# Kernel optimization log

Measured on AMD Instinct MI355X. Metric: run time of the kernel, lower is better.

## Reference

```python
import jax, jax.numpy as jnp
import numpy as np

N_NODES = 10000
N_EDGES = 160000
IN_FEAT = 1024
H_FEAT = 1024
NUM_CLASSES = 64


def setup_inputs() -> dict:
    key = jax.random.key(0)
    ks = jax.random.split(key, 8)
    h = jax.random.normal(ks[0], (N_NODES, IN_FEAT), dtype=jnp.float32)
    src = jax.random.randint(ks[1], (N_EDGES,), 0, N_NODES, dtype=jnp.int32)
    dst = jax.random.randint(ks[2], (N_EDGES,), 0, N_NODES, dtype=jnp.int32)
    # Xavier-ish scaled weights (DGL uses xavier_uniform for GraphConv)
    W1 = jax.random.normal(ks[3], (IN_FEAT, H_FEAT), dtype=jnp.float32) * (1.0 / np.sqrt(IN_FEAT))
    b1 = jnp.zeros((H_FEAT,), dtype=jnp.float32)
    W2 = jax.random.normal(ks[4], (H_FEAT, H_FEAT), dtype=jnp.float32) * (1.0 / np.sqrt(H_FEAT))
    b2 = jnp.zeros((H_FEAT,), dtype=jnp.float32)
    W3 = jax.random.normal(ks[5], (H_FEAT, NUM_CLASSES), dtype=jnp.float32) * (1.0 / np.sqrt(H_FEAT))
    b3 = jnp.zeros((NUM_CLASSES,), dtype=jnp.float32)
    return {"h": h, "src": src, "dst": dst,
            "W1": W1, "b1": b1, "W2": W2, "b2": b2, "W3": W3, "b3": b3}


def _graph_conv(src, dst, norm_src, norm_dst, x, W, b):
    """DGL GraphConv with norm='both':
    out = D_dst^{-1/2} * sum_{(u,v) in E} (D_src^{-1/2} * x)_u  @ W + b
    """
    xs = x * norm_src[:, None]                     # [N, d] scaled source feats
    msg = xs[src]                                  # [E, d] gather
    agg = jax.ops.segment_sum(msg, dst, num_segments=N_NODES)  # [N, d] scatter-add
    agg = agg * norm_dst[:, None]
    return agg @ W + b


def reference(h, src, dst, W1, b1, W2, b2, W3, b3):
    ones = jnp.ones((N_EDGES,), dtype=jnp.float32)
    deg_out = jax.ops.segment_sum(ones, src, num_segments=N_NODES)  # out-degree of src
    deg_in = jax.ops.segment_sum(ones, dst, num_segments=N_NODES)   # in-degree of dst
    norm_src = jnp.clip(deg_out, 1.0, None) ** -0.5
    norm_dst = jnp.clip(deg_in, 1.0, None) ** -0.5

    x = _graph_conv(src, dst, norm_src, norm_dst, h, W1, b1)
    x = jax.nn.relu(x)
    x = _graph_conv(src, dst, norm_src, norm_dst, x, W2, b2)
    x = jax.nn.relu(x)
    x = _graph_conv(src, dst, norm_src, norm_dst, x, W3, b3)
    return x
```

## Files before the change

### kernel.cpp

```cpp
#include <hip/hip_runtime.h>

constexpr int NN   = 10000;
constexpr int NE   = 160000;
constexpr int F    = 1024;
constexpr int C3   = 64;
constexpr int MPAD = 10240;

typedef __attribute__((ext_vector_type(8))) short short8;
typedef __attribute__((ext_vector_type(8))) unsigned short ushort8v;
typedef __attribute__((ext_vector_type(4))) float floatx4;

__device__ __forceinline__ unsigned short f2bf(float f) {
    union { float f; unsigned u; } v; v.f = f;
    unsigned r = v.u + 0x7fff + ((v.u >> 16) & 1);
    return (unsigned short)(r >> 16);
}
__device__ __forceinline__ float bf2f(unsigned short u) {
    union { unsigned u; float f; } v; v.u = ((unsigned)u) << 16;
    return v.f;
}

__device__ __forceinline__ void gl_lds16(const void* g, void* l) {
    __builtin_amdgcn_global_load_lds(
        (const __attribute__((address_space(1))) unsigned int*)g,
        (__attribute__((address_space(3))) unsigned int*)l, 16, 0, 0);
}


__global__ __launch_bounds__(256) void k_degree(const int* __restrict__ src,
                                                const int* __restrict__ dst,
                                                int* __restrict__ deg_out,
                                                int* __restrict__ deg_in) {
    int e = blockIdx.x * 256 + threadIdx.x;
    if (e < NE) {
        atomicAdd(&deg_out[src[e]], 1);
        atomicAdd(&deg_in[dst[e]], 1);
    }
}

__global__ __launch_bounds__(1024) void k_scan(const int* __restrict__ deg_in,
                                               const int* __restrict__ deg_out,
                                               int* __restrict__ row_ptr,
                                               int* __restrict__ cursor,
                                               float* __restrict__ norm_src,
                                               float* __restrict__ norm_dst) {
    constexpr int CH = 10;
    __shared__ int sums[1024];
    const int tid = threadIdx.x;
    int local[CH];
    int tsum = 0;
#pragma unroll
    for (int j = 0; j < CH; ++j) {
        int idx = tid * CH + j;
        int v = (idx < NN) ? deg_in[idx] : 0;
        local[j] = v;
        tsum += v;
        if (idx < MPAD) {
            norm_src[idx] = rsqrtf(fmaxf((float)deg_out[idx], 1.0f));
            norm_dst[idx] = rsqrtf(fmaxf((float)deg_in[idx], 1.0f));
        }
    }
    sums[tid] = tsum;
    __syncthreads();
    for (int off = 1; off < 1024; off <<= 1) {
        int v = (tid >= off) ? sums[tid - off] : 0;
        __syncthreads();
        sums[tid] += v;
        __syncthreads();
    }
    int run = sums[tid] - tsum;
#pragma unroll
    for (int j = 0; j < CH; ++j) {
        int idx = tid * CH + j;
        if (idx < NN) {
            row_ptr[idx] = run;
            cursor[idx]  = run;
        }
        run += local[j];
    }
    if (tid == 1023) row_ptr[NN] = sums[1023];
}

__global__ __launch_bounds__(256) void k_bucket(const int* __restrict__ src,
                                                const int* __restrict__ dst,
                                                int* __restrict__ cursor,
                                                int* __restrict__ csr_src) {
    int e = blockIdx.x * 256 + threadIdx.x;
    if (e < NE) {
        int slot = atomicAdd(&cursor[dst[e]], 1);
        csr_src[slot] = src[e];
    }
}

__global__ __launch_bounds__(256) void k_wconv_all(const float* __restrict__ W1,
                                                   const float* __restrict__ W2,
                                                   const float* __restrict__ W3,
                                                   unsigned short* __restrict__ Wt1,
                                                   unsigned short* __restrict__ Wt2,
                                                   unsigned short* __restrict__ Wt3) {
    __shared__ float tile[32][33];
    const float* W; unsigned short* Wt; int N, n0, k0;
    int b = blockIdx.x;
    if (b < 1024)      { W = W1; Wt = Wt1; N = F;  n0 = (b & 31) * 32;          k0 = (b >> 5) * 32; }
    else if (b < 2048) { b -= 1024; W = W2; Wt = Wt2; N = F;  n0 = (b & 31) * 32; k0 = (b >> 5) * 32; }
    else               { b -= 2048; W = W3; Wt = Wt3; N = C3; n0 = (b & 1) * 32;  k0 = (b >> 1) * 32; }
    const int tx = threadIdx.x & 31, ty = threadIdx.x >> 5;
#pragma unroll
    for (int i = 0; i < 32; i += 8)
        tile[ty + i][tx] = W[(size_t)(k0 + ty + i) * N + n0 + tx];
    __syncthreads();
#pragma unroll
    for (int i = 0; i < 32; i += 8)
        Wt[(size_t)(n0 + ty + i) * F + k0 + tx] = f2bf(tile[tx][ty + i]);
}


__global__ __launch_bounds__(256) void k_hcvt(const float* __restrict__ h,
                                              const float* __restrict__ norm_src,
                                              unsigned short* __restrict__ hb) {
    int idx = blockIdx.x * 256 + threadIdx.x;
    int v = idx >> 7, f8 = (idx & 127) * 8;
    float ns = norm_src[v];
    const float4 a = *(const float4*)(h + (size_t)v * F + f8);
    const float4 b = *(const float4*)(h + (size_t)v * F + f8 + 4);
    ushort8v o;
    o[0] = f2bf(ns * a.x); o[1] = f2bf(ns * a.y);
    o[2] = f2bf(ns * a.z); o[3] = f2bf(ns * a.w);
    o[4] = f2bf(ns * b.x); o[5] = f2bf(ns * b.y);
    o[6] = f2bf(ns * b.z); o[7] = f2bf(ns * b.w);
    *(ushort8v*)(hb + (size_t)v * F + f8) = o;
}

__global__ __launch_bounds__(256) void k_aggb(const unsigned short* __restrict__ xb,
                                              const int* __restrict__ row_ptr,
                                              const int* __restrict__ csr_src,
                                              unsigned short* __restrict__ aggb) {
    const int c = blockIdx.x & 7;
    const int g = blockIdx.x >> 3;
    const int v = g * 16 + (threadIdx.x >> 4);
    const int f8 = c * 128 + (threadIdx.x & 15) * 8;
    const unsigned short* xr = xb + f8;
    const int lo = row_ptr[v], hi = row_ptr[v + 1];
    float acc[8] = {0.f, 0.f, 0.f, 0.f, 0.f, 0.f, 0.f, 0.f};
    int i = lo;
    for (; i + 8 <= hi; i += 8) {
        int s0 = csr_src[i],     s1 = csr_src[i + 1];
        int s2 = csr_src[i + 2], s3 = csr_src[i + 3];
        int s4 = csr_src[i + 4], s5 = csr_src[i + 5];
        int s6 = csr_src[i + 6], s7 = csr_src[i + 7];
        ushort8v x0 = *(const ushort8v*)(xr + (size_t)s0 * F);
        ushort8v x1 = *(const ushort8v*)(xr + (size_t)s1 * F);
        ushort8v x2 = *(const ushort8v*)(xr + (size_t)s2 * F);
        ushort8v x3 = *(const ushort8v*)(xr + (size_t)s3 * F);
        ushort8v x4 = *(const ushort8v*)(xr + (size_t)s4 * F);
        ushort8v x5 = *(const ushort8v*)(xr + (size_t)s5 * F);
        ushort8v x6 = *(const ushort8v*)(xr + (size_t)s6 * F);
        ushort8v x7 = *(const ushort8v*)(xr + (size_t)s7 * F);
#pragma unroll
        for (int j = 0; j < 8; ++j) acc[j] += bf2f(x0[j]);
#pragma unroll
        for (int j = 0; j < 8; ++j) acc[j] += bf2f(x1[j]);
#pragma unroll
        for (int j = 0; j < 8; ++j) acc[j] += bf2f(x2[j]);
#pragma unroll
        for (int j = 0; j < 8; ++j) acc[j] += bf2f(x3[j]);
#pragma unroll
        for (int j = 0; j < 8; ++j) acc[j] += bf2f(x4[j]);
#pragma unroll
        for (int j = 0; j < 8; ++j) acc[j] += bf2f(x5[j]);
#pragma unroll
        for (int j = 0; j < 8; ++j) acc[j] += bf2f(x6[j]);
#pragma unroll
        for (int j = 0; j < 8; ++j) acc[j] += bf2f(x7[j]);
    }
    for (; i < hi; ++i) {
        int s = csr_src[i];
        ushort8v xv = *(const ushort8v*)(xr + (size_t)s * F);
#pragma unroll
        for (int j = 0; j < 8; ++j) acc[j] += bf2f(xv[j]);
    }
    ushort8v o;
#pragma unroll
    for (int j = 0; j < 8; ++j) o[j] = f2bf(acc[j]);
    *(ushort8v*)(aggb + (size_t)v * F + f8) = o;
}

__global__ __launch_bounds__(256) void k_agg64(const float* __restrict__ z,
                                               const int* __restrict__ row_ptr,
                                               const int* __restrict__ csr_src,
                                               const float* __restrict__ norm_dst,
                                               const float* __restrict__ b3,
                                               float* __restrict__ out) {
    const int v = blockIdx.x * 16 + (threadIdx.x >> 4);
    if (v >= NN) return;
    const int f4 = (threadIdx.x & 15) * 4;
    const int lo = row_ptr[v], hi = row_ptr[v + 1];
    float4 acc = {0.f, 0.f, 0.f, 0.f};
    int i = lo;
    for (; i + 4 <= hi; i += 4) {
        int s0 = csr_src[i],     s1 = csr_src[i + 1];
        int s2 = csr_src[i + 2], s3 = csr_src[i + 3];
        float4 z0 = *(const float4*)(z + (size_t)s0 * C3 + f4);
        float4 z1 = *(const float4*)(z + (size_t)s1 * C3 + f4);
        float4 z2 = *(const float4*)(z + (size_t)s2 * C3 + f4);
        float4 z3v = *(const float4*)(z + (size_t)s3 * C3 + f4);
        acc.x += z0.x + z1.x + z2.x + z3v.x;
        acc.y += z0.y + z1.y + z2.y + z3v.y;
        acc.z += z0.z + z1.z + z2.z + z3v.z;
        acc.w += z0.w + z1.w + z2.w + z3v.w;
    }
    for (; i < hi; ++i) {
        int s = csr_src[i];
        float4 zv = *(const float4*)(z + (size_t)s * C3 + f4);
        acc.x += zv.x; acc.y += zv.y; acc.z += zv.z; acc.w += zv.w;
    }
    float nd = norm_dst[v];
    float4 bv = *(const float4*)(b3 + f4);
    float4 o;
    o.x = acc.x * nd + bv.x; o.y = acc.y * nd + bv.y;
    o.z = acc.z * nd + bv.z; o.w = acc.w * nd + bv.w;
    *(float4*)(out + (size_t)v * C3 + f4) = o;
}

__global__ __launch_bounds__(512) void k_gemm_bf16(
        const unsigned short* __restrict__ A,
        const unsigned short* __restrict__ Bt,
        const float* __restrict__ bias,
        const float* __restrict__ rs1,
        const float* __restrict__ rs2,
        unsigned short* __restrict__ Cb) {
    __shared__ short As[3][128 * 32];
    __shared__ short Bs[3][128 * 32];
    const int t = threadIdx.x, lane = t & 63, wid = t >> 6;
    const int j = blockIdx.x >> 3;
    const int m0 = ((blockIdx.x & 7) * 10 + (j >> 3)) * 128;
    const int n0 = (j & 7) * 128;
    const int wm0 = (wid & 1) * 64, wn0 = (wid >> 1) * 32;
    const int lr = lane & 15, q = lane >> 4;

    const int rS  = wid * 16 + (lane >> 2);
    const int sS  = (((lane & 3) ^ ((rS >> 1) & 3)) * 8);
    const unsigned short* aSrc = A  + (size_t)(m0 + rS) * F + sS;
    const unsigned short* bSrc = Bt + (size_t)(n0 + rS) * F + sS;
    short* aDst = &As[0][wid * 512];
    short* bDst = &Bs[0][wid * 512];

    const short* ap[4];
    const short* bp[2];
#pragma unroll
    for (int mb = 0; mb < 4; ++mb) {
        int m = wm0 + mb * 16 + lr;
        ap[mb] = &As[0][m * 32 + (q ^ ((m >> 1) & 3)) * 8];
    }
#pragma unroll
    for (int nb = 0; nb < 2; ++nb) {
        int n = wn0 + nb * 16 + lr;
        bp[nb] = &Bs[0][n * 32 + (q ^ ((n >> 1) & 3)) * 8];
    }

    floatx4 acc[4][2] = {};

    gl_lds16(aSrc,      aDst);
    gl_lds16(bSrc,      bDst);
    gl_lds16(aSrc + 32, aDst + 4096);
    gl_lds16(bSrc + 32, bDst + 4096);

#pragma unroll
    for (int kt = 0; kt < F / 32; ++kt) {
        if (kt < F / 32 - 1) {
            asm volatile("s_waitcnt vmcnt(2)" ::: "memory");
        } else {
            asm volatile("s_waitcnt vmcnt(0)" ::: "memory");
        }
        __builtin_amdgcn_s_barrier();
        __builtin_amdgcn_sched_barrier(0);
        if (kt + 2 < F / 32) {
            const int k0 = (kt + 2) * 32;
            const int bb = ((kt + 2) % 3) * 4096;
            gl_lds16(aSrc + k0, aDst + bb);
            gl_lds16(bSrc + k0, bDst + bb);
        }
        const int bo = (kt % 3) * 4096;
        short8 af[4], bf[2];
#pragma unroll
        for (int mb = 0; mb < 4; ++mb) af[mb] = *(const short8*)(ap[mb] + bo);
#pragma unroll
        for (int nb = 0; nb < 2; ++nb) bf[nb] = *(const short8*)(bp[nb] + bo);
#pragma unroll
        for (int mb = 0; mb < 4; ++mb)
#pragma unroll
            for (int nb = 0; nb < 2; ++nb)
                acc[mb][nb] = __builtin_amdgcn_mfma_f32_16x16x32_bf16(
                    af[mb], bf[nb], acc[mb][nb], 0, 0, 0);
    }

    float s1[4][4], s2[4][4];
#pragma unroll
    for (int mb = 0; mb < 4; ++mb)
#pragma unroll
        for (int r = 0; r < 4; ++r) {
            int row = m0 + wm0 + mb * 16 + q * 4 + r;
            s1[mb][r] = rs1[row];
            s2[mb][r] = rs2[row];
        }
#pragma unroll
    for (int nb = 0; nb < 2; ++nb) {
        int col = n0 + wn0 + nb * 16 + lr;
        float bv = bias[col];
#pragma unroll
        for (int mb = 0; mb < 4; ++mb)
#pragma unroll
            for (int r = 0; r < 4; ++r) {
                int row = m0 + wm0 + mb * 16 + q * 4 + r;
                float v = fmaxf(acc[mb][nb][r] * s1[mb][r] + bv, 0.f) * s2[mb][r];
                Cb[(size_t)row * F + col] = f2bf(v);
            }
    }
}

__global__ __launch_bounds__(256) void k_gemm3(
        const unsigned short* __restrict__ A,
        const unsigned short* __restrict__ Bt,
        float* __restrict__ Z) {
    __shared__ short As3[2][64 * 32];
    __shared__ short Bs3[2][64 * 32];
    const int t = threadIdx.x, lane = t & 63, wid = t >> 6;
    const int m0 = blockIdx.x * 64;
    const int lr = lane & 15, q = lane >> 4;

    const int r = wid * 16 + (lane >> 2);
    const int soff = (((lane & 3) ^ ((r >> 1) & 3)) * 8);
    const unsigned short* aSrc = A  + (size_t)(m0 + r) * F + soff;
    const unsigned short* bSrc = Bt + (size_t)r * F + soff;

    const short* ap;
    {
        int m = wid * 16 + lr;
        ap = &As3[0][m * 32 + (q ^ ((m >> 1) & 3)) * 8];
    }
    const short* bp[4];
#pragma unroll
    for (int nb = 0; nb < 4; ++nb) {
        int n = nb * 16 + lr;
        bp[nb] = &Bs3[0][n * 32 + (q ^ ((n >> 1) & 3)) * 8];
    }

    floatx4 acc[4] = {};

    gl_lds16(aSrc, &As3[0][wid * 512]);
    gl_lds16(bSrc, &Bs3[0][wid * 512]);

    for (int kt = 0; kt < F / 32; ++kt) {
        const int buf = kt & 1;
        __syncthreads();
        if (kt + 1 < F / 32) {
            int k0 = (kt + 1) * 32;
            gl_lds16(aSrc + k0, &As3[buf ^ 1][wid * 512]);
            gl_lds16(bSrc + k0, &Bs3[buf ^ 1][wid * 512]);
        }
        const int bo = buf * (64 * 32);
        short8 af = *(const short8*)(ap + bo);
        short8 bf[4];
#pragma unroll
        for (int nb = 0; nb < 4; ++nb) bf[nb] = *(const short8*)(bp[nb] + bo);
#pragma unroll
        for (int nb = 0; nb < 4; ++nb)
            acc[nb] = __builtin_amdgcn_mfma_f32_16x16x32_bf16(af, bf[nb], acc[nb], 0, 0, 0);
    }

#pragma unroll
    for (int nb = 0; nb < 4; ++nb) {
        int col = nb * 16 + lr;
#pragma unroll
        for (int ri = 0; ri < 4; ++ri) {
            int row = m0 + wid * 16 + q * 4 + ri;
            Z[(size_t)row * C3 + col] = acc[nb][ri];
        }
    }
}


extern "C" void kernel_launch(void* const* d_in, const int* in_sizes, int n_in,
                              void* d_out, int out_size, void* d_ws, size_t ws_size,
                              hipStream_t stream) {
    const float* h   = (const float*)d_in[0];
    const int*   src = (const int*)d_in[1];
    const int*   dst = (const int*)d_in[2];
    const float* W1  = (const float*)d_in[3];
    const float* b1  = (const float*)d_in[4];
    const float* W2  = (const float*)d_in[5];
    const float* b2  = (const float*)d_in[6];
    const float* W3  = (const float*)d_in[7];
    const float* b3  = (const float*)d_in[8];
    float* out = (float*)d_out;

    char* ws = (char*)d_ws;
    int*   deg_out  = (int*)ws;                       ws += MPAD * 4;
    int*   deg_in   = (int*)ws;                       ws += MPAD * 4;
    float* norm_src = (float*)ws;                     ws += MPAD * 4;
    float* norm_dst = (float*)ws;                     ws += MPAD * 4;
    int*   row_ptr  = (int*)ws;                       ws += (NN + 1) * 4;
    int*   cursor   = (int*)ws;                       ws += NN * 4;
    int*   csr_src  = (int*)ws;                       ws += NE * 4;
    ws = (char*)(((size_t)ws + 255) & ~(size_t)255);
    unsigned short* hb   = (unsigned short*)ws;       ws += (size_t)MPAD * F * 2;
    unsigned short* aggb = (unsigned short*)ws;       ws += (size_t)MPAD * F * 2;
    unsigned short* xb   = (unsigned short*)ws;       ws += (size_t)MPAD * F * 2;
    unsigned short* Wt1  = (unsigned short*)ws;       ws += (size_t)F * F * 2;
    unsigned short* Wt2  = (unsigned short*)ws;       ws += (size_t)F * F * 2;
    unsigned short* Wt3  = (unsigned short*)ws;       ws += (size_t)C3 * F * 2;
    float* z3       = (float*)ws;

    hipMemsetAsync(deg_out, 0, 2 * MPAD * sizeof(int), stream);
    k_degree<<<(NE + 255) / 256, 256, 0, stream>>>(src, dst, deg_out, deg_in);
    k_scan<<<1, 1024, 0, stream>>>(deg_in, deg_out, row_ptr, cursor, norm_src, norm_dst);
    k_bucket<<<(NE + 255) / 256, 256, 0, stream>>>(src, dst, cursor, csr_src);
    k_wconv_all<<<2112, 256, 0, stream>>>(W1, W2, W3, Wt1, Wt2, Wt3);
    k_hcvt<<<NN * 128 / 256, 256, 0, stream>>>(h, norm_src, hb);

    k_aggb<<<(NN / 16) * 8, 256, 0, stream>>>(hb, row_ptr, csr_src, aggb);
    k_gemm_bf16<<<(MPAD / 128) * (F / 128), 512, 0, stream>>>(aggb, Wt1, b1, norm_dst, norm_src, xb);

    k_aggb<<<(NN / 16) * 8, 256, 0, stream>>>(xb, row_ptr, csr_src, aggb);
    k_gemm_bf16<<<(MPAD / 128) * (F / 128), 512, 0, stream>>>(aggb, Wt2, b2, norm_dst, norm_src, xb);

    k_gemm3<<<MPAD / 64, 256, 0, stream>>>(xb, Wt3, z3);
    k_agg64<<<(NN + 15) / 16, 256, 0, stream>>>(z3, row_ptr, csr_src, norm_dst, b3, out);
}
```

Before: 292.2 us.

## Switch bf16 GEMM to double-buffered 64-wide K tiles with 8-way swizzle

```diff
diff --git a/kernel.cpp b/kernel.cpp
--- a/kernel.cpp
+++ b/kernel.cpp
@@ -229,8 +229,8 @@
         const float* __restrict__ rs1,
         const float* __restrict__ rs2,
         unsigned short* __restrict__ Cb) {
-    __shared__ short As[3][128 * 32];
-    __shared__ short Bs[3][128 * 32];
+    __shared__ short As[2][128 * 64];
+    __shared__ short Bs[2][128 * 64];
     const int t = threadIdx.x, lane = t & 63, wid = t >> 6;
     const int j = blockIdx.x >> 3;
     const int m0 = ((blockIdx.x & 7) * 10 + (j >> 3)) * 128;
@@ -238,60 +238,69 @@
     const int wm0 = (wid & 1) * 64, wn0 = (wid >> 1) * 32;
     const int lr = lane & 15, q = lane >> 4;
 
-    const int rS  = wid * 16 + (lane >> 2);
-    const int sS  = (((lane & 3) ^ ((rS >> 1) & 3)) * 8);
+    const int rS = wid * 16 + (lane >> 3);
+    const int sS = (((lane & 7) ^ (rS & 7)) * 8);
     const unsigned short* aSrc = A  + (size_t)(m0 + rS) * F + sS;
     const unsigned short* bSrc = Bt + (size_t)(n0 + rS) * F + sS;
-    short* aDst = &As[0][wid * 512];
-    short* bDst = &Bs[0][wid * 512];
-
+    short* aDst = &As[0][wid * 1024];
+    short* bDst = &Bs[0][wid * 1024];
+
+    const int dk = (lr & 4) ? -32 : 32;
     const short* ap[4];
     const short* bp[2];
 #pragma unroll
     for (int mb = 0; mb < 4; ++mb) {
         int m = wm0 + mb * 16 + lr;
-        ap[mb] = &As[0][m * 32 + (q ^ ((m >> 1) & 3)) * 8];
+        ap[mb] = &As[0][m * 64 + ((q ^ (m & 7)) * 8)];
     }
 #pragma unroll
     for (int nb = 0; nb < 2; ++nb) {
         int n = wn0 + nb * 16 + lr;
-        bp[nb] = &Bs[0][n * 32 + (q ^ ((n >> 1) & 3)) * 8];
+        bp[nb] = &Bs[0][n * 64 + ((q ^ (n & 7)) * 8)];
     }
 
     floatx4 acc[4][2] = {};
 
-    gl_lds16(aSrc,      aDst);
-    gl_lds16(bSrc,      bDst);
-    gl_lds16(aSrc + 32, aDst + 4096);
-    gl_lds16(bSrc + 32, bDst + 4096);
-
-#pragma unroll
-    for (int kt = 0; kt < F / 32; ++kt) {
-        if (kt < F / 32 - 1) {
-            asm volatile("s_waitcnt vmcnt(2)" ::: "memory");
-        } else {
-            asm volatile("s_waitcnt vmcnt(0)" ::: "memory");
-        }
-        __builtin_amdgcn_s_barrier();
-        __builtin_amdgcn_sched_barrier(0);
-        if (kt + 2 < F / 32) {
-            const int k0 = (kt + 2) * 32;
-            const int bb = ((kt + 2) % 3) * 4096;
-            gl_lds16(aSrc + k0, aDst + bb);
-            gl_lds16(bSrc + k0, bDst + bb);
-        }
-        const int bo = (kt % 3) * 4096;
-        short8 af[4], bf[2];
-#pragma unroll
-        for (int mb = 0; mb < 4; ++mb) af[mb] = *(const short8*)(ap[mb] + bo);
-#pragma unroll
-        for (int nb = 0; nb < 2; ++nb) bf[nb] = *(const short8*)(bp[nb] + bo);
+    gl_lds16(aSrc,         aDst);
+    gl_lds16(aSrc + 8 * F, aDst + 512);
+    gl_lds16(bSrc,         bDst);
+    gl_lds16(bSrc + 8 * F, bDst + 512);
+
+    for (int kt = 0; kt < F / 64; ++kt) {
+        const int buf = kt & 1;
+        __syncthreads();
+        if (kt + 1 < F / 64) {
+            int k0 = (kt + 1) * 64;
+            int bb = (buf ^ 1) * (128 * 64);
+            gl_lds16(aSrc + k0,         aDst + bb);
+            gl_lds16(aSrc + 8 * F + k0, aDst + bb + 512);
+            gl_lds16(bSrc + k0,         bDst + bb);
+            gl_lds16(bSrc + 8 * F + k0, bDst + bb + 512);
+        }
+        const int bo = buf * (128 * 64);
+        short8 af0[4], af1[4], bf0[2], bf1[2];
+#pragma unroll
+        for (int mb = 0; mb < 4; ++mb) {
+            af0[mb] = *(const short8*)(ap[mb] + bo);
+            af1[mb] = *(const short8*)(ap[mb] + bo + dk);
+        }
+#pragma unroll
+        for (int nb = 0; nb < 2; ++nb) {
+            bf0[nb] = *(const short8*)(bp[nb] + bo);
+            bf1[nb] = *(const short8*)(bp[nb] + bo + dk);
+        }
 #pragma unroll
         for (int mb = 0; mb < 4; ++mb)
 #pragma unroll
             for (int nb = 0; nb < 2; ++nb)
                 acc[mb][nb] = __builtin_amdgcn_mfma_f32_16x16x32_bf16(
-                    af[mb], bf[nb], acc[mb][nb], 0, 0, 0);
+                    af0[mb], bf0[nb], acc[mb][nb], 0, 0, 0);
+#pragma unroll
+        for (int mb = 0; mb < 4; ++mb)
+#pragma unroll
+            for (int nb = 0; nb < 2; ++nb)
+                acc[mb][nb] = __builtin_amdgcn_mfma_f32_16x16x32_bf16(
+                    af1[mb], bf1[nb], acc[mb][nb], 0, 0, 0);
     }
 
     float s1[4][4], s2[4][4];
```

Measured after the change: 324.6 us. +11.1%, slower.
